# Kernel tuning notes

Hardware: AMD Instinct MI355X
Metric: run time of the kernel (lower is better)

The kernel has to match this reference:

```python
import jax, jax.numpy as jnp
import numpy as np

N_NODES = 100000
N_EDGES = 1600000
IN_DIM = 128
HID = 128


def sage_conv(x, src, dst, W_l, W_r, b, num_nodes):
    # PyG SAGEConv (mean aggregation): out = lin_l(mean_{j in N(i)} x_j) + lin_r(x_i)
    msgs = x[src]                                            # [E, F] gather
    agg = jax.ops.segment_sum(msgs, dst, num_segments=num_nodes)  # [N, F]
    cnt = jax.ops.segment_sum(jnp.ones((src.shape[0],), x.dtype), dst,
                              num_segments=num_nodes)        # [N]
    agg = agg / jnp.maximum(cnt, 1.0)[:, None]               # mean; 0 for isolated nodes
    return agg @ W_l + b + x @ W_r


def setup_inputs() -> dict:
    key = jax.random.key(0)
    ks = jax.random.split(key, 12)
    s_in = 1.0 / np.sqrt(IN_DIM)
    s_h = 1.0 / np.sqrt(HID)
    return {
        "x": jax.random.normal(ks[0], (N_NODES, IN_DIM), jnp.float32),
        "edge_index": jax.random.randint(ks[1], (2, N_EDGES), 0, N_NODES, jnp.int64),
        "Wl1": jax.random.normal(ks[2], (IN_DIM, HID), jnp.float32) * s_in,
        "Wr1": jax.random.normal(ks[3], (IN_DIM, HID), jnp.float32) * s_in,
        "b1": jnp.zeros((HID,), jnp.float32),
        "Wl2": jax.random.normal(ks[4], (HID, HID), jnp.float32) * s_h,
        "Wr2": jax.random.normal(ks[5], (HID, HID), jnp.float32) * s_h,
        "b2": jnp.zeros((HID,), jnp.float32),
        "Wp": jax.random.normal(ks[6], (HID, 1), jnp.float32) * s_h,
        "bp": jnp.zeros((1,), jnp.float32),
        "Wd": jax.random.normal(ks[7], (HID, 1), jnp.float32) * s_h,
        "bd": jnp.zeros((1,), jnp.float32),
    }


def reference(x, edge_index, Wl1, Wr1, b1, Wl2, Wr2, b2, Wp, bp, Wd, bd):
    src, dst = edge_index[0], edge_index[1]
    h = jax.nn.relu(sage_conv(x, src, dst, Wl1, Wr1, b1, N_NODES))
    h = jax.nn.relu(sage_conv(h, src, dst, Wl2, Wr2, b2, N_NODES))
    preds = h @ Wp + bp                      # [N, 1]
    diffs = jax.nn.sigmoid(h @ Wd + bd)      # [N, 1]
    return (preds - diffs, preds + diffs)
```

## Files before the change

### kernel.cpp

```cpp
#include <hip/hip_runtime.h>
#include <hip/hip_bf16.h>

#define N_NODES 100000
#define N_EDGES 1600000
#define NBUCK 391
#define BCAP 5120
#define ACHUNK 4096

typedef __bf16 bf16x8 __attribute__((ext_vector_type(8)));
typedef __bf16 bf16x4 __attribute__((ext_vector_type(4)));
typedef float  f32x4  __attribute__((ext_vector_type(4)));
typedef float  f32x2  __attribute__((ext_vector_type(2)));



__global__ __launch_bounds__(512) void zerob_kernel(int* __restrict__ bcnt,
                                                    int* __restrict__ P1s,
                                                    int* __restrict__ P2s) {
  int t = threadIdx.x;
  if (t < NBUCK) bcnt[t] = 0;
  if (t >= 480) { P1s[t - 480] = 0; P2s[t - 480] = 0; }
}

__global__ __launch_bounds__(256) void partA_kernel(const int* __restrict__ src,
                                                    const int* __restrict__ dst,
                                                    int* __restrict__ bcnt,
                                                    unsigned* __restrict__ packed, int E) {
  __shared__ int hist[NBUCK];
  __shared__ int curs[NBUCK];
  const int t = threadIdx.x;
  for (int i = t; i < NBUCK; i += 256) hist[i] = 0;
  __syncthreads();

  const int base = blockIdx.x * ACHUNK;
  const int lim = min(base + ACHUNK, E);

  int dloc[16], sloc[16];
  int myn = 0;
  for (int i = base + t; i < lim; i += 256) {
    dloc[myn] = dst[i];
    sloc[myn] = src[i];
    ++myn;
  }
  for (int k = 0; k < myn; ++k) atomicAdd(&hist[dloc[k] >> 8], 1);
  __syncthreads();

  for (int i = t; i < NBUCK; i += 256) {
    int h = hist[i];
    curs[i] = (h > 0) ? atomicAdd(&bcnt[i], h) : 0;
  }
  __syncthreads();

  for (int k = 0; k < myn; ++k) {
    int d = dloc[k];
    int b = d >> 8;
    int pos = atomicAdd(&curs[b], 1);
    if (pos < BCAP)
      packed[(size_t)b * BCAP + pos] = ((unsigned)sloc[k] << 8) | (unsigned)(d & 255);
  }
}

__global__ __launch_bounds__(256) void partBh_kernel(const unsigned* __restrict__ packed,
                                                     const int* __restrict__ bcnt,
                                                     int* __restrict__ pcnt,
                                                     int* __restrict__ deg,
                                                     int* __restrict__ pbt, int N) {
  __shared__ int hist[256];
  __shared__ int red[256];
  const int b = blockIdx.x, t = threadIdx.x;
  hist[t] = 0;
  __syncthreads();
  const int ecnt = min(bcnt[b], BCAP);
  const unsigned* pk = packed + (size_t)b * BCAP;
  for (int i = t; i < ecnt; i += 256) atomicAdd(&hist[pk[i] & 255u], 1);
  __syncthreads();
  int c = hist[t];
  int node = b * 256 + t;
  int pc = (node < N) ? ((c + 3) & ~3) : 0;
  if (node < N) { deg[node] = c; pcnt[node] = pc; }
  red[t] = pc;
  __syncthreads();
  for (int d = 128; d > 0; d >>= 1) {
    if (t < d) red[t] += red[t + d];
    __syncthreads();
  }
  if (t == 0) pbt[b] = red[0];
}

__global__ __launch_bounds__(512) void bscan_kernel(const int* __restrict__ pbt,
                                                    int* __restrict__ bbase,
                                                    int* __restrict__ offs, int N) {
  __shared__ int tmp[512];
  int t = threadIdx.x;
  int v = (t < NBUCK) ? pbt[t] : 0;
  int x = v;
  tmp[t] = x;
  __syncthreads();
  for (int d = 1; d < 512; d <<= 1) {
    int y = (t >= d) ? tmp[t - d] : 0;
    __syncthreads();
    x += y;
    tmp[t] = x;
    __syncthreads();
  }
  if (t < NBUCK) bbase[t] = x - v;
  if (t == NBUCK - 1) offs[N] = x;
}

__global__ __launch_bounds__(256) void partBs_kernel(const unsigned* __restrict__ packed,
                                                     const int* __restrict__ bcnt,
                                                     const int* __restrict__ bbase,
                                                     const int* __restrict__ pcnt,
                                                     const int* __restrict__ deg,
                                                     int* __restrict__ offs,
                                                     int* __restrict__ ssrc, int N) {
  __shared__ int scanbuf[256];
  __shared__ int curs[256];
  const int b = blockIdx.x, t = threadIdx.x;
  const int node = b * 256 + t;
  int pc = (node < N) ? pcnt[node] : 0;
  int c  = (node < N) ? deg[node] : 0;
  int x = pc;
  scanbuf[t] = x;
  __syncthreads();
  for (int d = 1; d < 256; d <<= 1) {
    int y = (t >= d) ? scanbuf[t - d] : 0;
    __syncthreads();
    x += y;
    scanbuf[t] = x;
    __syncthreads();
  }
  int excl = x - pc;
  const int obase = bbase[b];
  if (node < N) offs[node] = obase + excl;
  curs[t] = excl;
  __syncthreads();

  const int ecnt = min(bcnt[b], BCAP);
  const unsigned* pk = packed + (size_t)b * BCAP;
  for (int i = t; i < ecnt; i += 256) {
    unsigned p = pk[i];
    int r = atomicAdd(&curs[p & 255u], 1);
    ssrc[obase + r] = (int)(p >> 8);
  }
  for (int j = c; j < pc; ++j) ssrc[obase + excl + j] = N;
}


__global__ __launch_bounds__(256) void wswz_kernel(const float* __restrict__ Wl1,
                                                   const float* __restrict__ Wr1,
                                                   const float* __restrict__ Wl2,
                                                   const float* __restrict__ Wr2,
                                                   __bf16* __restrict__ W1out,
                                                   __bf16* __restrict__ W2out) {
  int gi = blockIdx.x * blockDim.x + threadIdx.x;
  bool L2 = gi >= 32768;
  int i = gi & 32767;
  int j = i & 7;
  int lane = (i >> 3) & 63;
  int c = (i >> 9) & 3;
  int tile = i >> 11;
  int k = c * 32 + ((lane >> 4) * 8) + j;
  int krow = L2 ? (((k & 7) << 4) | (k >> 3)) : k;
  int col = tile * 16 + (lane & 15);
  const float* Wl = L2 ? Wl2 : Wl1;
  const float* Wr = L2 ? Wr2 : Wr1;
  float v = (col < 128) ? Wl[krow * 128 + col] : Wr[krow * 128 + (col - 128)];
  (L2 ? W2out : W1out)[i] = (__bf16)v;
}


__global__ __launch_bounds__(256, 2) void gemm1_kernel(const float* __restrict__ A,
                                                       const __bf16* __restrict__ Wswz,
                                                       const float* __restrict__ bias,
                                                       unsigned char* __restrict__ P,
                                                       __bf16* __restrict__ R, int M,
                                                       int tiles, int stride) {
  __shared__ __bf16 ldsA[64][136];
  const int t = threadIdx.x;
  const int lane = t & 63;
  const int w = t >> 6;
  const int q = lane >> 4;
  const int s = lane & 15;

  bf16x8 bfrag[16];
#pragma unroll
  for (int ct = 0; ct < 4; ++ct)
#pragma unroll
    for (int c = 0; c < 4; ++c)
      bfrag[ct * 4 + c] =
          *(const bf16x8*)&Wswz[(size_t)((((w * 4 + ct) * 4 + c) * 64) + lane) * 8];

  float breg[4];
#pragma unroll
  for (int j = 0; j < 4; ++j)
    breg[j] = (w >= 2) ? bias[((w - 2) * 4 + j) * 16 + s] : 0.f;

  for (int tile = blockIdx.x; tile < tiles; tile += stride) {
    const int m0 = tile * 64;

#pragma unroll
    for (int it = 0; it < 8; ++it) {
      int row = it * 8 + (t >> 5);
      int col = (t & 31) * 4;
      float4 v = make_float4(0.f, 0.f, 0.f, 0.f);
      if (m0 + row < M) v = *(const float4*)&A[(size_t)(m0 + row) * 128 + col];
      bf16x4 bv;
      bv.x = (__bf16)v.x; bv.y = (__bf16)v.y; bv.z = (__bf16)v.z; bv.w = (__bf16)v.w;
      *(bf16x4*)&ldsA[row][col] = bv;
    }
    __syncthreads();

    bf16x8 afrag[16];
#pragma unroll
    for (int rt = 0; rt < 4; ++rt)
#pragma unroll
      for (int c = 0; c < 4; ++c)
        afrag[rt * 4 + c] = *(const bf16x8*)&ldsA[rt * 16 + s][c * 32 + q * 8];

    f32x4 acc[16];
    f32x4 zero = {0.f, 0.f, 0.f, 0.f};
#pragma unroll
    for (int i = 0; i < 16; ++i) acc[i] = zero;

#pragma unroll
    for (int c = 0; c < 4; ++c)
#pragma unroll
      for (int rt = 0; rt < 4; ++rt)
#pragma unroll
        for (int ct = 0; ct < 4; ++ct)
          acc[rt * 4 + ct] = __builtin_amdgcn_mfma_f32_16x16x32_bf16(
              afrag[rt * 4 + c], bfrag[ct * 4 + c], acc[rt * 4 + ct], 0, 0, 0);

#pragma unroll
    for (int rt = 0; rt < 4; ++rt) {
#pragma unroll
      for (int r = 0; r < 4; ++r) {
        int row = m0 + rt * 16 + q * 4 + r;
        if (row < M) {
          if (w < 2) {
            unsigned v = 0;
            v = __builtin_amdgcn_cvt_pk_fp8_f32(acc[rt * 4 + 0][r], acc[rt * 4 + 1][r], v, false);
            v = __builtin_amdgcn_cvt_pk_fp8_f32(acc[rt * 4 + 2][r], acc[rt * 4 + 3][r], v, true);
            *(unsigned*)&P[(size_t)row * 128 + s * 8 + w * 4] = v;
          } else {
            bf16x4 o;
#pragma unroll
            for (int ct = 0; ct < 4; ++ct) o[ct] = (__bf16)(acc[rt * 4 + ct][r] + breg[ct]);
            *(bf16x4*)&R[(size_t)row * 128 + s * 8 + (w - 2) * 4] = o;
          }
        }
      }
    }
    __syncthreads();
  }
}


__global__ __launch_bounds__(256, 2) void fused_kernel(
    const unsigned char* __restrict__ P1, __bf16* R,
    const int* __restrict__ offs, const int* __restrict__ deg,
    const int* __restrict__ ssrc,
    const __bf16* __restrict__ Wswz, const float* __restrict__ bias,
    unsigned char* __restrict__ P2, int n, int ntiles, int stride) {
  __shared__ __bf16 ldsH[16][136];
  const int t = threadIdx.x;
  const int lane = t & 63;
  const int w = t >> 6;
  const int q = lane >> 4;
  const int s = lane & 15;

  bf16x8 bfrag[16];
#pragma unroll
  for (int ct = 0; ct < 4; ++ct)
#pragma unroll
    for (int c = 0; c < 4; ++c)
      bfrag[ct * 4 + c] =
          *(const bf16x8*)&Wswz[(size_t)((((w * 4 + ct) * 4 + c) * 64) + lane) * 8];

  float breg[4];
#pragma unroll
  for (int j = 0; j < 4; ++j)
    breg[j] = (w >= 2) ? bias[((w - 2) * 4 + j) * 16 + s] : 0.f;

  const unsigned char* Pb = P1 + (size_t)s * 8;

  for (int tile = blockIdx.x; tile < ntiles; tile += stride) {
    int node = tile * 16 + w * 4 + q;
    int nc = min(node, n - 1);
    int start = offs[nc];
    int pend = offs[nc + 1];

    f32x2 a01 = {0.f, 0.f}, a23 = {0.f, 0.f}, a45 = {0.f, 0.f}, a67 = {0.f, 0.f};
    for (int cur = start; cur < pend; cur += 8) {
      uint4 sv = *(const uint4*)&ssrc[cur];
      uint2 v0 = *(const uint2*)(Pb + (size_t)sv.x * 128);
      uint2 v1 = *(const uint2*)(Pb + (size_t)sv.y * 128);
      uint2 v2 = *(const uint2*)(Pb + (size_t)sv.z * 128);
      uint2 v3 = *(const uint2*)(Pb + (size_t)sv.w * 128);
      if (cur + 4 < pend) {
        uint4 sw = *(const uint4*)&ssrc[cur + 4];
        uint2 u0 = *(const uint2*)(Pb + (size_t)sw.x * 128);
        uint2 u1 = *(const uint2*)(Pb + (size_t)sw.y * 128);
        uint2 u2 = *(const uint2*)(Pb + (size_t)sw.z * 128);
        uint2 u3 = *(const uint2*)(Pb + (size_t)sw.w * 128);
        a01 += __builtin_amdgcn_cvt_pk_f32_fp8(u0.x, false);
        a23 += __builtin_amdgcn_cvt_pk_f32_fp8(u0.x, true);
        a45 += __builtin_amdgcn_cvt_pk_f32_fp8(u0.y, false);
        a67 += __builtin_amdgcn_cvt_pk_f32_fp8(u0.y, true);
        a01 += __builtin_amdgcn_cvt_pk_f32_fp8(u1.x, false);
        a23 += __builtin_amdgcn_cvt_pk_f32_fp8(u1.x, true);
        a45 += __builtin_amdgcn_cvt_pk_f32_fp8(u1.y, false);
        a67 += __builtin_amdgcn_cvt_pk_f32_fp8(u1.y, true);
        a01 += __builtin_amdgcn_cvt_pk_f32_fp8(u2.x, false);
        a23 += __builtin_amdgcn_cvt_pk_f32_fp8(u2.x, true);
        a45 += __builtin_amdgcn_cvt_pk_f32_fp8(u2.y, false);
        a67 += __builtin_amdgcn_cvt_pk_f32_fp8(u2.y, true);
        a01 += __builtin_amdgcn_cvt_pk_f32_fp8(u3.x, false);
        a23 += __builtin_amdgcn_cvt_pk_f32_fp8(u3.x, true);
        a45 += __builtin_amdgcn_cvt_pk_f32_fp8(u3.y, false);
        a67 += __builtin_amdgcn_cvt_pk_f32_fp8(u3.y, true);
      }
      a01 += __builtin_amdgcn_cvt_pk_f32_fp8(v0.x, false);
      a23 += __builtin_amdgcn_cvt_pk_f32_fp8(v0.x, true);
      a45 += __builtin_amdgcn_cvt_pk_f32_fp8(v0.y, false);
      a67 += __builtin_amdgcn_cvt_pk_f32_fp8(v0.y, true);
      a01 += __builtin_amdgcn_cvt_pk_f32_fp8(v1.x, false);
      a23 += __builtin_amdgcn_cvt_pk_f32_fp8(v1.x, true);
      a45 += __builtin_amdgcn_cvt_pk_f32_fp8(v1.y, false);
      a67 += __builtin_amdgcn_cvt_pk_f32_fp8(v1.y, true);
      a01 += __builtin_amdgcn_cvt_pk_f32_fp8(v2.x, false);
      a23 += __builtin_amdgcn_cvt_pk_f32_fp8(v2.x, true);
      a45 += __builtin_amdgcn_cvt_pk_f32_fp8(v2.y, false);
      a67 += __builtin_amdgcn_cvt_pk_f32_fp8(v2.y, true);
      a01 += __builtin_amdgcn_cvt_pk_f32_fp8(v3.x, false);
      a23 += __builtin_amdgcn_cvt_pk_f32_fp8(v3.x, true);
      a45 += __builtin_amdgcn_cvt_pk_f32_fp8(v3.y, false);
      a67 += __builtin_amdgcn_cvt_pk_f32_fp8(v3.y, true);
    }

    int dg = deg[nc];
    float inv = 1.0f / (float)(dg > 0 ? dg : 1);
    bf16x8 rv = *(const bf16x8*)&R[(size_t)nc * 128 + s * 8];
    float acc1[8] = {a01[0], a01[1], a23[0], a23[1], a45[0], a45[1], a67[0], a67[1]};
    bf16x8 hh;
#pragma unroll
    for (int j = 0; j < 8; ++j)
      hh[j] = (__bf16)fmaxf(acc1[j] * inv + (float)rv[j], 0.f);

    *(bf16x8*)&ldsH[w * 4 + q][s * 8] = hh;
    __syncthreads();

    bf16x8 afrag[4];
#pragma unroll
    for (int c = 0; c < 4; ++c)
      afrag[c] = *(const bf16x8*)&ldsH[s][c * 32 + q * 8];

    f32x4 acc2[4];
    f32x4 zero = {0.f, 0.f, 0.f, 0.f};
#pragma unroll
    for (int i = 0; i < 4; ++i) acc2[i] = zero;

#pragma unroll
    for (int c = 0; c < 4; ++c)
#pragma unroll
      for (int ct = 0; ct < 4; ++ct)
        acc2[ct] = __builtin_amdgcn_mfma_f32_16x16x32_bf16(afrag[c], bfrag[ct * 4 + c],
                                                           acc2[ct], 0, 0, 0);

#pragma unroll
    for (int r = 0; r < 4; ++r) {
      int row = tile * 16 + q * 4 + r;
      if (row < n) {
        if (w < 2) {
          unsigned v = 0;
          v = __builtin_amdgcn_cvt_pk_fp8_f32(acc2[0][r], acc2[1][r], v, false);
          v = __builtin_amdgcn_cvt_pk_fp8_f32(acc2[2][r], acc2[3][r], v, true);
          *(unsigned*)&P2[(size_t)row * 128 + s * 8 + w * 4] = v;
        } else {
          bf16x4 o;
#pragma unroll
          for (int ct = 0; ct < 4; ++ct) o[ct] = (__bf16)(acc2[ct][r] + breg[ct]);
          *(bf16x4*)&R[(size_t)row * 128 + s * 8 + (w - 2) * 4] = o;
        }
      }
    }
    __syncthreads();
  }
}


__global__ __launch_bounds__(256) void agg2_kernel(
    const unsigned char* __restrict__ P, const __bf16* __restrict__ R,
    const int* __restrict__ offs, const int* __restrict__ deg,
    const int* __restrict__ ssrc, float* __restrict__ out,
    const float* __restrict__ Wp, const float* __restrict__ Wd,
    const float* __restrict__ bp, const float* __restrict__ bd, int n) {
  int w4 = (int)((blockIdx.x * blockDim.x + threadIdx.x) >> 6);
  int lane = threadIdx.x & 63;
  int g = lane >> 4;
  int s = lane & 15;
  int node = w4 * 4 + g;
  int nc = min(node, n - 1);
  int start = offs[nc];
  int pend = offs[nc + 1];

  f32x2 a01 = {0.f, 0.f}, a23 = {0.f, 0.f}, a45 = {0.f, 0.f}, a67 = {0.f, 0.f};

  const unsigned char* Pb = P + (size_t)s * 8;
  for (int cur = start; cur < pend; cur += 4) {
    uint4 sv = *(const uint4*)&ssrc[cur];
    uint2 v0 = *(const uint2*)(Pb + (size_t)sv.x * 128);
    uint2 v1 = *(const uint2*)(Pb + (size_t)sv.y * 128);
    uint2 v2 = *(const uint2*)(Pb + (size_t)sv.z * 128);
    uint2 v3 = *(const uint2*)(Pb + (size_t)sv.w * 128);
    a01 += __builtin_amdgcn_cvt_pk_f32_fp8(v0.x, false);
    a23 += __builtin_amdgcn_cvt_pk_f32_fp8(v0.x, true);
    a45 += __builtin_amdgcn_cvt_pk_f32_fp8(v0.y, false);
    a67 += __builtin_amdgcn_cvt_pk_f32_fp8(v0.y, true);
    a01 += __builtin_amdgcn_cvt_pk_f32_fp8(v1.x, false);
    a23 += __builtin_amdgcn_cvt_pk_f32_fp8(v1.x, true);
    a45 += __builtin_amdgcn_cvt_pk_f32_fp8(v1.y, false);
    a67 += __builtin_amdgcn_cvt_pk_f32_fp8(v1.y, true);
    a01 += __builtin_amdgcn_cvt_pk_f32_fp8(v2.x, false);
    a23 += __builtin_amdgcn_cvt_pk_f32_fp8(v2.x, true);
    a45 += __builtin_amdgcn_cvt_pk_f32_fp8(v2.y, false);
    a67 += __builtin_amdgcn_cvt_pk_f32_fp8(v2.y, true);
    a01 += __builtin_amdgcn_cvt_pk_f32_fp8(v3.x, false);
    a23 += __builtin_amdgcn_cvt_pk_f32_fp8(v3.x, true);
    a45 += __builtin_amdgcn_cvt_pk_f32_fp8(v3.y, false);
    a67 += __builtin_amdgcn_cvt_pk_f32_fp8(v3.y, true);
  }

  int dg = deg[nc];
  float inv = 1.0f / (float)(dg > 0 ? dg : 1);

  bf16x8 rv = *(const bf16x8*)&R[(size_t)nc * 128 + s * 8];
  float acc[8] = {a01[0], a01[1], a23[0], a23[1], a45[0], a45[1], a67[0], a67[1]};
  float p = 0.f, dd = 0.f;
#pragma unroll
  for (int j = 0; j < 8; ++j) {
    float h = fmaxf(acc[j] * inv + (float)rv[j], 0.f);
    p += h * Wp[j * 16 + s];
    dd += h * Wd[j * 16 + s];
  }
  p += __shfl_xor(p, 1, 64);  p += __shfl_xor(p, 2, 64);
  p += __shfl_xor(p, 4, 64);  p += __shfl_xor(p, 8, 64);
  dd += __shfl_xor(dd, 1, 64); dd += __shfl_xor(dd, 2, 64);
  dd += __shfl_xor(dd, 4, 64); dd += __shfl_xor(dd, 8, 64);
  if (node < n && s == 0) {
    float preds = p + bp[0];
    float sg = 1.0f / (1.0f + __expf(-(dd + bd[0])));
    out[node] = preds - sg;
    out[n + node] = preds + sg;
  }
}


extern "C" void kernel_launch(void* const* d_in, const int* in_sizes, int n_in,
                              void* d_out, int out_size, void* d_ws, size_t ws_size,
                              hipStream_t stream) {
  const float* x    = (const float*)d_in[0];
  const int*   ei   = (const int*)d_in[1];
  const float* Wl1 = (const float*)d_in[2];
  const float* Wr1 = (const float*)d_in[3];
  const float* b1  = (const float*)d_in[4];
  const float* Wl2 = (const float*)d_in[5];
  const float* Wr2 = (const float*)d_in[6];
  const float* b2  = (const float*)d_in[7];
  const float* Wp  = (const float*)d_in[8];
  const float* bp  = (const float*)d_in[9];
  const float* Wd  = (const float*)d_in[10];
  const float* bd  = (const float*)d_in[11];
  float* out = (float*)d_out;

  const int N = N_NODES, E = N_EDGES;
  const int* src = ei;
  const int* dst = ei + E;
  const size_t PADE = (size_t)E + 3 * (size_t)N + 64;

  char* w = (char*)d_ws;
  unsigned char* P1 = (unsigned char*)w; w += (size_t)(N + 1) * 128;
  unsigned char* P2 = (unsigned char*)w; w += (size_t)(N + 1) * 128;
  __bf16* Rbuf   = (__bf16*)w;   w += (size_t)N * 128 * 2;
  int* ssrc      = (int*)w;      w += PADE * 4;
  unsigned* pck  = (unsigned*)w; w += (size_t)NBUCK * BCAP * 4;
  int* bcnt      = (int*)w;      w += 512 * 4;
  int* bbase     = (int*)w;      w += 512 * 4;
  int* pbt       = (int*)w;      w += 512 * 4;
  int* pcnt      = (int*)w;      w += (size_t)(N + 32) * 4;
  int* deg       = (int*)w;      w += (size_t)(N + 32) * 4;
  int* offs      = (int*)w;      w += (size_t)(N + 32) * 4;
  __bf16* Ws1    = (__bf16*)w;   w += 65536;
  __bf16* Ws2    = (__bf16*)w;   w += 65536;

  zerob_kernel<<<1, 512, 0, stream>>>(bcnt, (int*)(P1 + (size_t)N * 128),
                                      (int*)(P2 + (size_t)N * 128));
  wswz_kernel<<<256, 256, 0, stream>>>(Wl1, Wr1, Wl2, Wr2, Ws1, Ws2);
  partA_kernel<<<(E + ACHUNK - 1) / ACHUNK, 256, 0, stream>>>(src, dst, bcnt, pck, E);
  partBh_kernel<<<NBUCK, 256, 0, stream>>>(pck, bcnt, pcnt, deg, pbt, N);
  bscan_kernel<<<1, 512, 0, stream>>>(pbt, bbase, offs, N);
  partBs_kernel<<<NBUCK, 256, 0, stream>>>(pck, bcnt, bbase, pcnt, deg, offs, ssrc, N);

  const int TILES = (N + 63) / 64;
  const int NT16  = (N + 15) / 16;
  const int GG = 512;
  gemm1_kernel<<<GG, 256, 0, stream>>>(x, Ws1, b1, P1, Rbuf, N, TILES, GG);
  fused_kernel<<<GG, 256, 0, stream>>>(P1, Rbuf, offs, deg, ssrc, Ws2, b2, P2, N, NT16, GG);
  agg2_kernel<<<NT16, 256, 0, stream>>>(P2, Rbuf, offs, deg, ssrc, out,
                                        Wp, Wd, bp, bd, N);
}
```

Baseline: 278.6 us.

## Merge preprocessing kernels, overlap GEMM1 with edge bucketing, use 64-row fused tiles

```diff
diff --git a/kernel.cpp b/kernel.cpp
--- a/kernel.cpp
+++ b/kernel.cpp
@@ -6,6 +6,7 @@
 #define NBUCK 391
 #define BCAP 5120
 #define ACHUNK 4096
+#define GTILES 1563
 
 typedef __bf16 bf16x8 __attribute__((ext_vector_type(8)));
 typedef __bf16 bf16x4 __attribute__((ext_vector_type(4)));
@@ -14,146 +15,24 @@
 
 
 
-__global__ __launch_bounds__(512) void zerob_kernel(int* __restrict__ bcnt,
-                                                    int* __restrict__ P1s,
-                                                    int* __restrict__ P2s) {
-  int t = threadIdx.x;
-  if (t < NBUCK) bcnt[t] = 0;
-  if (t >= 480) { P1s[t - 480] = 0; P2s[t - 480] = 0; }
-}
-
-__global__ __launch_bounds__(256) void partA_kernel(const int* __restrict__ src,
-                                                    const int* __restrict__ dst,
-                                                    int* __restrict__ bcnt,
-                                                    unsigned* __restrict__ packed, int E) {
-  __shared__ int hist[NBUCK];
-  __shared__ int curs[NBUCK];
-  const int t = threadIdx.x;
-  for (int i = t; i < NBUCK; i += 256) hist[i] = 0;
-  __syncthreads();
-
-  const int base = blockIdx.x * ACHUNK;
-  const int lim = min(base + ACHUNK, E);
-
-  int dloc[16], sloc[16];
-  int myn = 0;
-  for (int i = base + t; i < lim; i += 256) {
-    dloc[myn] = dst[i];
-    sloc[myn] = src[i];
-    ++myn;
-  }
-  for (int k = 0; k < myn; ++k) atomicAdd(&hist[dloc[k] >> 8], 1);
-  __syncthreads();
-
-  for (int i = t; i < NBUCK; i += 256) {
-    int h = hist[i];
-    curs[i] = (h > 0) ? atomicAdd(&bcnt[i], h) : 0;
-  }
-  __syncthreads();
-
-  for (int k = 0; k < myn; ++k) {
-    int d = dloc[k];
-    int b = d >> 8;
-    int pos = atomicAdd(&curs[b], 1);
-    if (pos < BCAP)
-      packed[(size_t)b * BCAP + pos] = ((unsigned)sloc[k] << 8) | (unsigned)(d & 255);
-  }
-}
-
-__global__ __launch_bounds__(256) void partBh_kernel(const unsigned* __restrict__ packed,
-                                                     const int* __restrict__ bcnt,
-                                                     int* __restrict__ pcnt,
-                                                     int* __restrict__ deg,
-                                                     int* __restrict__ pbt, int N) {
-  __shared__ int hist[256];
-  __shared__ int red[256];
-  const int b = blockIdx.x, t = threadIdx.x;
-  hist[t] = 0;
-  __syncthreads();
-  const int ecnt = min(bcnt[b], BCAP);
-  const unsigned* pk = packed + (size_t)b * BCAP;
-  for (int i = t; i < ecnt; i += 256) atomicAdd(&hist[pk[i] & 255u], 1);
-  __syncthreads();
-  int c = hist[t];
-  int node = b * 256 + t;
-  int pc = (node < N) ? ((c + 3) & ~3) : 0;
-  if (node < N) { deg[node] = c; pcnt[node] = pc; }
-  red[t] = pc;
-  __syncthreads();
-  for (int d = 128; d > 0; d >>= 1) {
-    if (t < d) red[t] += red[t + d];
-    __syncthreads();
-  }
-  if (t == 0) pbt[b] = red[0];
-}
-
-__global__ __launch_bounds__(512) void bscan_kernel(const int* __restrict__ pbt,
-                                                    int* __restrict__ bbase,
-                                                    int* __restrict__ offs, int N) {
-  __shared__ int tmp[512];
-  int t = threadIdx.x;
-  int v = (t < NBUCK) ? pbt[t] : 0;
-  int x = v;
-  tmp[t] = x;
-  __syncthreads();
-  for (int d = 1; d < 512; d <<= 1) {
-    int y = (t >= d) ? tmp[t - d] : 0;
-    __syncthreads();
-    x += y;
-    tmp[t] = x;
-    __syncthreads();
-  }
-  if (t < NBUCK) bbase[t] = x - v;
-  if (t == NBUCK - 1) offs[N] = x;
-}
-
-__global__ __launch_bounds__(256) void partBs_kernel(const unsigned* __restrict__ packed,
-                                                     const int* __restrict__ bcnt,
-                                                     const int* __restrict__ bbase,
-                                                     const int* __restrict__ pcnt,
-                                                     const int* __restrict__ deg,
-                                                     int* __restrict__ offs,
-                                                     int* __restrict__ ssrc, int N) {
-  __shared__ int scanbuf[256];
-  __shared__ int curs[256];
-  const int b = blockIdx.x, t = threadIdx.x;
-  const int node = b * 256 + t;
-  int pc = (node < N) ? pcnt[node] : 0;
-  int c  = (node < N) ? deg[node] : 0;
-  int x = pc;
-  scanbuf[t] = x;
-  __syncthreads();
-  for (int d = 1; d < 256; d <<= 1) {
-    int y = (t >= d) ? scanbuf[t - d] : 0;
-    __syncthreads();
-    x += y;
-    scanbuf[t] = x;
-    __syncthreads();
-  }
-  int excl = x - pc;
-  const int obase = bbase[b];
-  if (node < N) offs[node] = obase + excl;
-  curs[t] = excl;
-  __syncthreads();
-
-  const int ecnt = min(bcnt[b], BCAP);
-  const unsigned* pk = packed + (size_t)b * BCAP;
-  for (int i = t; i < ecnt; i += 256) {
-    unsigned p = pk[i];
-    int r = atomicAdd(&curs[p & 255u], 1);
-    ssrc[obase + r] = (int)(p >> 8);
-  }
-  for (int j = c; j < pc; ++j) ssrc[obase + excl + j] = N;
-}
-
-
-__global__ __launch_bounds__(256) void wswz_kernel(const float* __restrict__ Wl1,
+__global__ __launch_bounds__(256) void init_kernel(int* __restrict__ bcnt,
+                                                   int* __restrict__ cursor,
+                                                   int* __restrict__ P1s,
+                                                   int* __restrict__ P2s,
+                                                   const float* __restrict__ Wl1,
                                                    const float* __restrict__ Wr1,
                                                    const float* __restrict__ Wl2,
                                                    const float* __restrict__ Wr2,
                                                    __bf16* __restrict__ W1out,
                                                    __bf16* __restrict__ W2out) {
-  int gi = blockIdx.x * blockDim.x + threadIdx.x;
+  const int b = blockIdx.x, t = threadIdx.x;
+  if (b == 0) {
+    for (int i = t; i < NBUCK; i += 256) bcnt[i] = 0;
+    if (t == 0) cursor[0] = 0;
+    if (t < 32) { P1s[t] = 0; P2s[t] = 0; }
+    return;
+  }
+  int gi = (b - 1) * 256 + t;
   bool L2 = gi >= 32768;
   int i = gi & 32767;
   int j = i & 7;
@@ -170,18 +49,196 @@
 }
 
 
-__global__ __launch_bounds__(256, 2) void gemm1_kernel(const float* __restrict__ A,
-                                                       const __bf16* __restrict__ Wswz,
-                                                       const float* __restrict__ bias,
-                                                       unsigned char* __restrict__ P,
-                                                       __bf16* __restrict__ R, int M,
-                                                       int tiles, int stride) {
+__global__ __launch_bounds__(256, 2) void work1_kernel(
+    const float* __restrict__ A, const __bf16* __restrict__ Wswz,
+    const float* __restrict__ bias, unsigned char* __restrict__ P,
+    __bf16* __restrict__ R, int M,
+    const int* __restrict__ src, const int* __restrict__ dst,
+    int* __restrict__ bcnt, unsigned* __restrict__ packed, int E) {
   __shared__ __bf16 ldsA[64][136];
+  __shared__ int hist[NBUCK];
+  __shared__ int curs[NBUCK];
+  const int t = threadIdx.x;
+
+  if (blockIdx.x >= GTILES) {
+    for (int i = t; i < NBUCK; i += 256) hist[i] = 0;
+    __syncthreads();
+
+    const int base = (blockIdx.x - GTILES) * ACHUNK;
+    const int lim = min(base + ACHUNK, E);
+
+    int dloc[16], sloc[16];
+    int myn = 0;
+    for (int i = base + t; i < lim; i += 256) {
+      dloc[myn] = dst[i];
+      sloc[myn] = src[i];
+      ++myn;
+    }
+    for (int k = 0; k < myn; ++k) atomicAdd(&hist[dloc[k] >> 8], 1);
+    __syncthreads();
+
+    for (int i = t; i < NBUCK; i += 256) {
+      int h = hist[i];
+      curs[i] = (h > 0) ? atomicAdd(&bcnt[i], h) : 0;
+    }
+    __syncthreads();
+
+    for (int k = 0; k < myn; ++k) {
+      int d = dloc[k];
+      int b = d >> 8;
+      int pos = atomicAdd(&curs[b], 1);
+      if (pos < BCAP)
+        packed[(size_t)b * BCAP + pos] = ((unsigned)sloc[k] << 8) | (unsigned)(d & 255);
+    }
+    return;
+  }
+
+  const int lane = t & 63;
+  const int w = t >> 6;
+  const int q = lane >> 4;
+  const int s = lane & 15;
+  const int m0 = blockIdx.x * 64;
+
+  bf16x8 bfrag[16];
+#pragma unroll
+  for (int ct = 0; ct < 4; ++ct)
+#pragma unroll
+    for (int c = 0; c < 4; ++c)
+      bfrag[ct * 4 + c] =
+          *(const bf16x8*)&Wswz[(size_t)((((w * 4 + ct) * 4 + c) * 64) + lane) * 8];
+
+#pragma unroll
+  for (int it = 0; it < 8; ++it) {
+    int row = it * 8 + (t >> 5);
+    int col = (t & 31) * 4;
+    float4 v = make_float4(0.f, 0.f, 0.f, 0.f);
+    if (m0 + row < M) v = *(const float4*)&A[(size_t)(m0 + row) * 128 + col];
+    bf16x4 bv;
+    bv.x = (__bf16)v.x; bv.y = (__bf16)v.y; bv.z = (__bf16)v.z; bv.w = (__bf16)v.w;
+    *(bf16x4*)&ldsA[row][col] = bv;
+  }
+
+  float breg[4];
+#pragma unroll
+  for (int j = 0; j < 4; ++j)
+    breg[j] = (w >= 2) ? bias[((w - 2) * 4 + j) * 16 + s] : 0.f;
+
+  __syncthreads();
+
+  bf16x8 afrag[16];
+#pragma unroll
+  for (int rt = 0; rt < 4; ++rt)
+#pragma unroll
+    for (int c = 0; c < 4; ++c)
+      afrag[rt * 4 + c] = *(const bf16x8*)&ldsA[rt * 16 + s][c * 32 + q * 8];
+
+  f32x4 acc[16];
+  f32x4 zero = {0.f, 0.f, 0.f, 0.f};
+#pragma unroll
+  for (int i = 0; i < 16; ++i) acc[i] = zero;
+
+#pragma unroll
+  for (int c = 0; c < 4; ++c)
+#pragma unroll
+    for (int rt = 0; rt < 4; ++rt)
+#pragma unroll
+      for (int ct = 0; ct < 4; ++ct)
+        acc[rt * 4 + ct] = __builtin_amdgcn_mfma_f32_16x16x32_bf16(
+            afrag[rt * 4 + c], bfrag[ct * 4 + c], acc[rt * 4 + ct], 0, 0, 0);
+
+#pragma unroll
+  for (int rt = 0; rt < 4; ++rt) {
+#pragma unroll
+    for (int r = 0; r < 4; ++r) {
+      int row = m0 + rt * 16 + q * 4 + r;
+      if (row < M) {
+        if (w < 2) {
+          unsigned v = 0;
+          v = __builtin_amdgcn_cvt_pk_fp8_f32(acc[rt * 4 + 0][r], acc[rt * 4 + 1][r], v, false);
+          v = __builtin_amdgcn_cvt_pk_fp8_f32(acc[rt * 4 + 2][r], acc[rt * 4 + 3][r], v, true);
+          *(unsigned*)&P[(size_t)row * 128 + s * 8 + w * 4] = v;
+        } else {
+          bf16x4 o;
+#pragma unroll
+          for (int ct = 0; ct < 4; ++ct) o[ct] = (__bf16)(acc[rt * 4 + ct][r] + breg[ct]);
+          *(bf16x4*)&R[(size_t)row * 128 + s * 8 + (w - 2) * 4] = o;
+        }
+      }
+    }
+  }
+}
+
+
+__global__ __launch_bounds__(256) void partB_kernel(const unsigned* __restrict__ packed,
+                                                    const int* __restrict__ bcnt,
+                                                    int* __restrict__ cursor,
+                                                    int* __restrict__ offs,
+                                                    int* __restrict__ deg,
+                                                    int* __restrict__ ssrc, int N) {
+  __shared__ int hist[256];
+  __shared__ int scanbuf[256];
+  __shared__ int curs[256];
+  __shared__ int sbase;
+  const int b = blockIdx.x, t = threadIdx.x;
+  const int nb = b * 256;
+  hist[t] = 0;
+  __syncthreads();
+
+  const int ecnt = min(bcnt[b], BCAP);
+  const unsigned* pk = packed + (size_t)b * BCAP;
+  unsigned ploc[20];
+  int myn = 0;
+  for (int i = t; i < ecnt; i += 256) {
+    unsigned p = pk[i];
+    ploc[myn++] = p;
+    atomicAdd(&hist[p & 255u], 1);
+  }
+  __syncthreads();
+
+  int c = hist[t];
+  int node = nb + t;
+  int pc = (node < N) ? ((c + 3) & ~3) : 0;
+  int x = pc;
+  scanbuf[t] = x;
+  __syncthreads();
+  for (int d = 1; d < 256; d <<= 1) {
+    int y = (t >= d) ? scanbuf[t - d] : 0;
+    __syncthreads();
+    x += y;
+    scanbuf[t] = x;
+    __syncthreads();
+  }
+  if (t == 255) sbase = atomicAdd(cursor, x);
+  __syncthreads();
+  const int base = sbase;
+  int excl = x - pc;
+  if (node < N) { offs[node] = base + excl; deg[node] = c; }
+  curs[t] = excl;
+  __syncthreads();
+
+  for (int k = 0; k < myn; ++k) {
+    unsigned p = ploc[k];
+    int r = atomicAdd(&curs[p & 255u], 1);
+    ssrc[base + r] = (int)(p >> 8);
+  }
+  for (int j = c; j < pc; ++j) ssrc[base + excl + j] = N;
+}
+
+
+__global__ __launch_bounds__(256, 2) void fusedA_kernel(
+    const unsigned char* __restrict__ P1, __bf16* R,
+    const int* __restrict__ offs, const int* __restrict__ deg,
+    const int* __restrict__ ssrc,
+    const __bf16* __restrict__ Wswz, const float* __restrict__ bias,
+    unsigned char* __restrict__ P2, int N) {
+  __shared__ __bf16 Hlds[64][136];
   const int t = threadIdx.x;
   const int lane = t & 63;
   const int w = t >> 6;
   const int q = lane >> 4;
-  const int s = lane & 15;
+  const int s = t & 15;
+  const int g = t >> 4;
+  const int nb = blockIdx.x * 64;
 
   bf16x8 bfrag[16];
 #pragma unroll
@@ -196,131 +253,23 @@
   for (int j = 0; j < 4; ++j)
     breg[j] = (w >= 2) ? bias[((w - 2) * 4 + j) * 16 + s] : 0.f;
 
-  for (int tile = blockIdx.x; tile < tiles; tile += stride) {
-    const int m0 = tile * 64;
-
-#pragma unroll
-    for (int it = 0; it < 8; ++it) {
-      int row = it * 8 + (t >> 5);
-      int col = (t & 31) * 4;
-      float4 v = make_float4(0.f, 0.f, 0.f, 0.f);
-      if (m0 + row < M) v = *(const float4*)&A[(size_t)(m0 + row) * 128 + col];
-      bf16x4 bv;
-      bv.x = (__bf16)v.x; bv.y = (__bf16)v.y; bv.z = (__bf16)v.z; bv.w = (__bf16)v.w;
-      *(bf16x4*)&ldsA[row][col] = bv;
-    }
-    __syncthreads();
-
-    bf16x8 afrag[16];
-#pragma unroll
-    for (int rt = 0; rt < 4; ++rt)
-#pragma unroll
-      for (int c = 0; c < 4; ++c)
-        afrag[rt * 4 + c] = *(const bf16x8*)&ldsA[rt * 16 + s][c * 32 + q * 8];
-
-    f32x4 acc[16];
-    f32x4 zero = {0.f, 0.f, 0.f, 0.f};
-#pragma unroll
-    for (int i = 0; i < 16; ++i) acc[i] = zero;
-
-#pragma unroll
-    for (int c = 0; c < 4; ++c)
-#pragma unroll
-      for (int rt = 0; rt < 4; ++rt)
-#pragma unroll
-        for (int ct = 0; ct < 4; ++ct)
-          acc[rt * 4 + ct] = __builtin_amdgcn_mfma_f32_16x16x32_bf16(
-              afrag[rt * 4 + c], bfrag[ct * 4 + c], acc[rt * 4 + ct], 0, 0, 0);
-
-#pragma unroll
-    for (int rt = 0; rt < 4; ++rt) {
-#pragma unroll
-      for (int r = 0; r < 4; ++r) {
-        int row = m0 + rt * 16 + q * 4 + r;
-        if (row < M) {
-          if (w < 2) {
-            unsigned v = 0;
-            v = __builtin_amdgcn_cvt_pk_fp8_f32(acc[rt * 4 + 0][r], acc[rt * 4 + 1][r], v, false);
-            v = __builtin_amdgcn_cvt_pk_fp8_f32(acc[rt * 4 + 2][r], acc[rt * 4 + 3][r], v, true);
-            *(unsigned*)&P[(size_t)row * 128 + s * 8 + w * 4] = v;
-          } else {
-            bf16x4 o;
-#pragma unroll
-            for (int ct = 0; ct < 4; ++ct) o[ct] = (__bf16)(acc[rt * 4 + ct][r] + breg[ct]);
-            *(bf16x4*)&R[(size_t)row * 128 + s * 8 + (w - 2) * 4] = o;
-          }
-        }
-      }
-    }
-    __syncthreads();
-  }
-}
-
-
-__global__ __launch_bounds__(256, 2) void fused_kernel(
-    const unsigned char* __restrict__ P1, __bf16* R,
-    const int* __restrict__ offs, const int* __restrict__ deg,
-    const int* __restrict__ ssrc,
-    const __bf16* __restrict__ Wswz, const float* __restrict__ bias,
-    unsigned char* __restrict__ P2, int n, int ntiles, int stride) {
-  __shared__ __bf16 ldsH[16][136];
-  const int t = threadIdx.x;
-  const int lane = t & 63;
-  const int w = t >> 6;
-  const int q = lane >> 4;
-  const int s = lane & 15;
-
-  bf16x8 bfrag[16];
-#pragma unroll
-  for (int ct = 0; ct < 4; ++ct)
-#pragma unroll
-    for (int c = 0; c < 4; ++c)
-      bfrag[ct * 4 + c] =
-          *(const bf16x8*)&Wswz[(size_t)((((w * 4 + ct) * 4 + c) * 64) + lane) * 8];
-
-  float breg[4];
-#pragma unroll
-  for (int j = 0; j < 4; ++j)
-    breg[j] = (w >= 2) ? bias[((w - 2) * 4 + j) * 16 + s] : 0.f;
-
   const unsigned char* Pb = P1 + (size_t)s * 8;
-
-  for (int tile = blockIdx.x; tile < ntiles; tile += stride) {
-    int node = tile * 16 + w * 4 + q;
-    int nc = min(node, n - 1);
+#pragma unroll
+  for (int k = 0; k < 4; ++k) {
+    int dl = g * 4 + k;
+    int node = nb + dl;
+    int nc = min(node, N - 1);
     int start = offs[nc];
-    int pend = offs[nc + 1];
+    int dg = deg[nc];
+    int pend = start + ((dg + 3) & ~3);
 
     f32x2 a01 = {0.f, 0.f}, a23 = {0.f, 0.f}, a45 = {0.f, 0.f}, a67 = {0.f, 0.f};
-    for (int cur = start; cur < pend; cur += 8) {
+    for (int cur = start; cur < pend; cur += 4) {
       uint4 sv = *(const uint4*)&ssrc[cur];
       uint2 v0 = *(const uint2*)(Pb + (size_t)sv.x * 128);
       uint2 v1 = *(const uint2*)(Pb + (size_t)sv.y * 128);
       uint2 v2 = *(const uint2*)(Pb + (size_t)sv.z * 128);
       uint2 v3 = *(const uint2*)(Pb + (size_t)sv.w * 128);
-      if (cur + 4 < pend) {
-        uint4 sw = *(const uint4*)&ssrc[cur + 4];
-        uint2 u0 = *(const uint2*)(Pb + (size_t)sw.x * 128);
-        uint2 u1 = *(const uint2*)(Pb + (size_t)sw.y * 128);
-        uint2 u2 = *(const uint2*)(Pb + (size_t)sw.z * 128);
-        uint2 u3 = *(const uint2*)(Pb + (size_t)sw.w * 128);
-        a01 += __builtin_amdgcn_cvt_pk_f32_fp8(u0.x, false);
-        a23 += __builtin_amdgcn_cvt_pk_f32_fp8(u0.x, true);
-        a45 += __builtin_amdgcn_cvt_pk_f32_fp8(u0.y, false);
-        a67 += __builtin_amdgcn_cvt_pk_f32_fp8(u0.y, true);
-        a01 += __builtin_amdgcn_cvt_pk_f32_fp8(u1.x, false);
-        a23 += __builtin_amdgcn_cvt_pk_f32_fp8(u1.x, true);
-        a45 += __builtin_amdgcn_cvt_pk_f32_fp8(u1.y, false);
-        a67 += __builtin_amdgcn_cvt_pk_f32_fp8(u1.y, true);
-        a01 += __builtin_amdgcn_cvt_pk_f32_fp8(u2.x, false);
-        a23 += __builtin_amdgcn_cvt_pk_f32_fp8(u2.x, true);
-        a45 += __builtin_amdgcn_cvt_pk_f32_fp8(u2.y, false);
-        a67 += __builtin_amdgcn_cvt_pk_f32_fp8(u2.y, true);
-        a01 += __builtin_amdgcn_cvt_pk_f32_fp8(u3.x, false);
-        a23 += __builtin_amdgcn_cvt_pk_f32_fp8(u3.x, true);
-        a45 += __builtin_amdgcn_cvt_pk_f32_fp8(u3.y, false);
-        a67 += __builtin_amdgcn_cvt_pk_f32_fp8(u3.y, true);
-      }
       a01 += __builtin_amdgcn_cvt_pk_f32_fp8(v0.x, false);
       a23 += __builtin_amdgcn_cvt_pk_f32_fp8(v0.x, true);
       a45 += __builtin_amdgcn_cvt_pk_f32_fp8(v0.y, false);
@@ -339,7 +288,6 @@
       a67 += __builtin_amdgcn_cvt_pk_f32_fp8(v3.y, true);
     }
 
-    int dg = deg[nc];
     float inv = 1.0f / (float)(dg > 0 ? dg : 1);
     bf16x8 rv = *(const bf16x8*)&R[(size_t)nc * 128 + s * 8];
     float acc1[8] = {a01[0], a01[1], a23[0], a23[1], a45[0], a45[1], a67[0], a67[1]};
@@ -347,45 +295,50 @@
 #pragma unroll
     for (int j = 0; j < 8; ++j)
       hh[j] = (__bf16)fmaxf(acc1[j] * inv + (float)rv[j], 0.f);
-
-    *(bf16x8*)&ldsH[w * 4 + q][s * 8] = hh;
-    __syncthreads();
-
-    bf16x8 afrag[4];
+    *(bf16x8*)&Hlds[dl][s * 8] = hh;
+  }
+  __syncthreads();
+
+  bf16x8 afrag[16];
+#pragma unroll
+  for (int rt = 0; rt < 4; ++rt)
 #pragma unroll
     for (int c = 0; c < 4; ++c)
-      afrag[c] = *(const bf16x8*)&ldsH[s][c * 32 + q * 8];
-
-    f32x4 acc2[4];
-    f32x4 zero = {0.f, 0.f, 0.f, 0.f};
-#pragma unroll
-    for (int i = 0; i < 4; ++i) acc2[i] = zero;
-
-#pragma unroll
-    for (int c = 0; c < 4; ++c)
+      afrag[rt * 4 + c] = *(const bf16x8*)&Hlds[rt * 16 + s][c * 32 + q * 8];
+
+  f32x4 acc[16];
+  f32x4 zero = {0.f, 0.f, 0.f, 0.f};
+#pragma unroll
+  for (int i = 0; i < 16; ++i) acc[i] = zero;
+
+#pragma unroll
+  for (int c = 0; c < 4; ++c)
+#pragma unroll
+    for (int rt = 0; rt < 4; ++rt)
 #pragma unroll
       for (int ct = 0; ct < 4; ++ct)
-        acc2[ct] = __builtin_amdgcn_mfma_f32_16x16x32_bf16(afrag[c], bfrag[ct * 4 + c],
-                                                           acc2[ct], 0, 0, 0);
-
+        acc[rt * 4 + ct] = __builtin_amdgcn_mfma_f32_16x16x32_bf16(
+            afrag[rt * 4 + c], bfrag[ct * 4 + c], acc[rt * 4 + ct], 0, 0, 0);
+
+#pragma unroll
+  for (int rt = 0; rt < 4; ++rt) {
 #pragma unroll
     for (int r = 0; r < 4; ++r) {
-      int row = tile * 16 + q * 4 + r;
-      if (row < n) {
+      int row = nb + rt * 16 + q * 4 + r;
+      if (row < N) {
         if (w < 2) {
           unsigned v = 0;
-          v = __builtin_amdgcn_cvt_pk_fp8_f32(acc2[0][r], acc2[1][r], v, false);
-          v = __builtin_amdgcn_cvt_pk_fp8_f32(acc2[2][r], acc2[3][r], v, true);
+          v = __builtin_amdgcn_cvt_pk_fp8_f32(acc[rt * 4 + 0][r], acc[rt * 4 + 1][r], v, false);
+          v = __builtin_amdgcn_cvt_pk_fp8_f32(acc[rt * 4 + 2][r], acc[rt * 4 + 3][r], v, true);
           *(unsigned*)&P2[(size_t)row * 128 + s * 8 + w * 4] = v;
         } else {
           bf16x4 o;
 #pragma unroll
-          for (int ct = 0; ct < 4; ++ct) o[ct] = (__bf16)(acc2[ct][r] + breg[ct]);
+          for (int ct = 0; ct < 4; ++ct) o[ct] = (__bf16)(acc[rt * 4 + ct][r] + breg[ct]);
           *(bf16x4*)&R[(size_t)row * 128 + s * 8 + (w - 2) * 4] = o;
         }
       }
     }
-    __syncthreads();
   }
 }
 
@@ -403,7 +356,8 @@
   int node = w4 * 4 + g;
   int nc = min(node, n - 1);
   int start = offs[nc];
-  int pend = offs[nc + 1];
+  int dg = deg[nc];
+  int pend = start + ((dg + 3) & ~3);
 
   f32x2 a01 = {0.f, 0.f}, a23 = {0.f, 0.f}, a45 = {0.f, 0.f}, a67 = {0.f, 0.f};
 
@@ -432,7 +386,6 @@
     a67 += __builtin_amdgcn_cvt_pk_f32_fp8(v3.y, true);
   }
 
-  int dg = deg[nc];
   float inv = 1.0f / (float)(dg > 0 ? dg : 1);
 
   bf16x8 rv = *(const bf16x8*)&R[(size_t)nc * 128 + s * 8];
@@ -486,27 +439,22 @@
   int* ssrc      = (int*)w;      w += PADE * 4;
   unsigned* pck  = (unsigned*)w; w += (size_t)NBUCK * BCAP * 4;
   int* bcnt      = (int*)w;      w += 512 * 4;
-  int* bbase     = (int*)w;      w += 512 * 4;
-  int* pbt       = (int*)w;      w += 512 * 4;
-  int* pcnt      = (int*)w;      w += (size_t)(N + 32) * 4;
+  int* cursor    = (int*)w;      w += 64 * 4;
   int* deg       = (int*)w;      w += (size_t)(N + 32) * 4;
   int* offs      = (int*)w;      w += (size_t)(N + 32) * 4;
   __bf16* Ws1    = (__bf16*)w;   w += 65536;
   __bf16* Ws2    = (__bf16*)w;   w += 65536;
 
-  zerob_kernel<<<1, 512, 0, stream>>>(bcnt, (int*)(P1 + (size_t)N * 128),
-                                      (int*)(P2 + (size_t)N * 128));
-  wswz_kernel<<<256, 256, 0, stream>>>(Wl1, Wr1, Wl2, Wr2, Ws1, Ws2);
-  partA_kernel<<<(E + ACHUNK - 1) / ACHUNK, 256, 0, stream>>>(src, dst, bcnt, pck, E);
-  partBh_kernel<<<NBUCK, 256, 0, stream>>>(pck, bcnt, pcnt, deg, pbt, N);
-  bscan_kernel<<<1, 512, 0, stream>>>(pbt, bbase, offs, N);
-  partBs_kernel<<<NBUCK, 256, 0, stream>>>(pck, bcnt, bbase, pcnt, deg, offs, ssrc, N);
-
-  const int TILES = (N + 63) / 64;
-  const int NT16  = (N + 15) / 16;
-  const int GG = 512;
-  gemm1_kernel<<<GG, 256, 0, stream>>>(x, Ws1, b1, P1, Rbuf, N, TILES, GG);
-  fused_kernel<<<GG, 256, 0, stream>>>(P1, Rbuf, offs, deg, ssrc, Ws2, b2, P2, N, NT16, GG);
-  agg2_kernel<<<NT16, 256, 0, stream>>>(P2, Rbuf, offs, deg, ssrc, out,
-                                        Wp, Wd, bp, bd, N);
-}
+  const int PABLK = (E + ACHUNK - 1) / ACHUNK;
+
+  init_kernel<<<257, 256, 0, stream>>>(bcnt, cursor,
+                                       (int*)(P1 + (size_t)N * 128),
+                                       (int*)(P2 + (size_t)N * 128),
+                                       Wl1, Wr1, Wl2, Wr2, Ws1, Ws2);
+  work1_kernel<<<GTILES + PABLK, 256, 0, stream>>>(x, Ws1, b1, P1, Rbuf, N,
+                                                   src, dst, bcnt, pck, E);
+  partB_kernel<<<NBUCK, 256, 0, stream>>>(pck, bcnt, cursor, offs, deg, ssrc, N);
+  fusedA_kernel<<<GTILES, 256, 0, stream>>>(P1, Rbuf, offs, deg, ssrc, Ws2, b2, P2, N);
+  agg2_kernel<<<(N + 15) / 16, 256, 0, stream>>>(P2, Rbuf, offs, deg, ssrc, out,
+                                                 Wp, Wd, bp, bd, N);
+}
```

Result: faster. 270.5 us (-2.9%).
